# Kernel optimization log

Measured on AMD Instinct MI355X. Metric: run time of the kernel, lower is better.

Reference implementation:

```python
import jax, jax.numpy as jnp
import numpy as np

B = 32          # batch_size
S = 64          # num_subgraph
D = 8           # dim_multi_hot (module-level global in source repo)
NE = S * D      # num_edges = 512
NNODES = 1024
E = 150000      # incidence rows
IN_UNITS = [16, 32, 32]
OUT_UNITS = [32, 32, 16]


def _glorot(key, shape):
    # glorot_normal over last two dims (out, in)
    fan_out, fan_in = shape[-2], shape[-1]
    std = (2.0 / (fan_in + fan_out)) ** 0.5
    return std * jax.random.normal(key, shape, dtype=jnp.float32)


def setup_inputs() -> dict:
    key = jax.random.key(0)
    ks = jax.random.split(key, 10)
    nodes_features = jax.random.normal(ks[0], (NNODES * S, IN_UNITS[0]), dtype=jnp.float32)
    c0 = jax.random.randint(ks[1], (E,), 0, B, dtype=jnp.int32)
    c1 = jax.random.randint(ks[2], (E,), 0, NNODES, dtype=jnp.int32)
    c2 = jax.random.randint(ks[3], (E,), 0, S, dtype=jnp.int32)
    c3 = jax.random.randint(ks[4], (E,), 0, D, dtype=jnp.int32)
    incidence_matrix = jnp.stack([c0, c1, c2, c3], axis=1)
    return {
        'nodes_features': nodes_features,
        'in_core0': _glorot(ks[5], (NE, IN_UNITS[1], IN_UNITS[0])),
        'in_bias0': jnp.zeros((NE, IN_UNITS[1], 1), jnp.float32),
        'in_core1': _glorot(ks[6], (NE, IN_UNITS[2], IN_UNITS[1])),
        'in_bias1': jnp.zeros((NE, IN_UNITS[2], 1), jnp.float32),
        'out_core0': _glorot(ks[7], (NE, OUT_UNITS[1], OUT_UNITS[0])),
        'out_bias0': jnp.zeros((NE, OUT_UNITS[1], 1), jnp.float32),
        'out_core1': _glorot(ks[8], (NE, OUT_UNITS[2], OUT_UNITS[1])),
        'out_bias1': jnp.zeros((NE, OUT_UNITS[2], 1), jnp.float32),
        'incidence_matrix': incidence_matrix,
    }


def reference(nodes_features, in_core0, in_bias0, in_core1, in_bias1,
              out_core0, out_bias0, out_core1, out_bias1, incidence_matrix):
    c0 = incidence_matrix[:, 0]
    c1 = incidence_matrix[:, 1]
    c2 = incidence_matrix[:, 2]
    c3 = incidence_matrix[:, 3]

    # gather node features per incidence row: [E, in0]
    x = nodes_features[c1 * S + c2]
    eidx = c2 * D + c3  # per-edge weight index, < NE

    # per-edge MLP (gathered batched matmul + bias + relu)
    for W, b in ((in_core0, in_bias0), (in_core1, in_bias1)):
        x = jax.nn.relu(jnp.einsum('eoi,ei->eo', W[eidx], x) + b[eidx, :, 0])

    # unsorted segment mean over irregular edge groups
    seg = c0 * (D * S) + c2 * D + c3
    nseg = B * S * D
    sums = jax.ops.segment_sum(x, seg, num_segments=nseg)           # [B*NE, 32]
    cnt = jax.ops.segment_sum(jnp.ones((x.shape[0], 1), x.dtype), seg, num_segments=nseg)
    ef = jnp.where(cnt > 0, sums / jnp.maximum(cnt, 1.0), 0.0)       # [B*NE, 32]

    # output MLP: weights tiled over batch (einsum avoids explicit repeat)
    ef = ef.reshape(B, NE, -1)
    for W, b in ((out_core0, out_bias0), (out_core1, out_bias1)):
        ef = jax.nn.relu(jnp.einsum('eoi,bei->beo', W, ef) + b[None, :, :, 0])

    return ef.reshape(B * NE, OUT_UNITS[-1], 1)
```

## Files before the change

### kernel.cpp

```cpp
#include <hip/hip_runtime.h>

#define B_    32
#define S_    64
#define D_    8
#define NE_   512
#define E_    150000
#define CAP   448

#define SBLK  1024
#define BLKN  ((E_ + SBLK - 1) / SBLK)
#define SLOTS 16
#define PBIN_PITCH (BLKN * SLOTS)

#define PAYLOAD_BYTE_OFF (NE_ * BLKN * 4)

typedef __attribute__((ext_vector_type(8)))  short  short8;
typedef __attribute__((ext_vector_type(16))) float  float16;

__device__ __forceinline__ unsigned short f2bf(float f) {
    union { float f; unsigned int u; } cv; cv.f = f;
    unsigned int u = cv.u;
    return (unsigned short)((u + 0x7fffu + ((u >> 16) & 1u)) >> 16);
}
__device__ __forceinline__ unsigned int pack2bf(float a, float b) {
    return (unsigned int)f2bf(a) | ((unsigned int)f2bf(b) << 16);
}

__global__ __launch_bounds__(SBLK)
void scatter_bin(const int* __restrict__ inc,
                 int* __restrict__ cnt2D,
                 int* __restrict__ payload2D) {
    __shared__ int lcount[NE_];
    const int tid = threadIdx.x;

    for (int i = tid; i < NE_; i += SBLK) lcount[i] = 0;
    __syncthreads();

    const int e = blockIdx.x * SBLK + tid;
    int ei = -1, lp = 0, pl = 0;
    if (e < E_) {
        const int4 c = ((const int4*)inc)[e];
        ei = c.z * D_ + c.w;
        pl = (c.x << 16) | (c.y * S_ + c.z);
        lp = atomicAdd(&lcount[ei], 1);
    }
    if (ei >= 0 && lp < SLOTS)
        payload2D[ei * PBIN_PITCH + blockIdx.x * SLOTS + lp] = pl;
    __syncthreads();
    if (tid < NE_)
        cnt2D[tid * BLKN + blockIdx.x] = min(lcount[tid], SLOTS);
}

#define HLP 40

__global__ __launch_bounds__(512, 4)
void main_mfma(const float* __restrict__ nf,
               const float* __restrict__ iw0, const float* __restrict__ ib0,
               const float* __restrict__ iw1, const float* __restrict__ ib1,
               const float* __restrict__ ow0, const float* __restrict__ ob0,
               const float* __restrict__ ow1, const float* __restrict__ ob1,
               const int* __restrict__ cnt2D, const int* __restrict__ payload2D,
               float* __restrict__ out) {
    const int bid  = blockIdx.x;
    const int tid  = threadIdx.x;
    const int lane = tid & 63;
    const int wav  = tid >> 6;
    const int e32  = lane & 31;
    const int q    = lane >> 5;

    __shared__ float acc[32][33];
    __shared__ float hb[32][33];
    __shared__ float cnts[32];
    __shared__ float q0t[32 * 33];
    __shared__ float q1t[32 * 17];
    __shared__ float qb0s[32], qb1s[16];
    __shared__ float bias0s[32], bias1s[32];
    __shared__ int   scnt[160];
    __shared__ int   elist[CAP];
    __shared__ unsigned short Hl[8][32 * HLP];

    short8 aWa, aWb0, aWb1;
    {
        const float* wa = iw0 + (size_t)bid * 512 + e32 * 16 + q * 8;
        float4 u0 = ((const float4*)wa)[0], u1 = ((const float4*)wa)[1];
        unsigned int p[4] = { pack2bf(u0.x,u0.y), pack2bf(u0.z,u0.w),
                              pack2bf(u1.x,u1.y), pack2bf(u1.z,u1.w) };
        aWa = *(short8*)p;
    }
    {
        const float* wb = iw1 + (size_t)bid * 1024 + e32 * 32 + q * 8;
        float4 u0 = ((const float4*)wb)[0], u1 = ((const float4*)wb)[1];
        unsigned int p[4] = { pack2bf(u0.x,u0.y), pack2bf(u0.z,u0.w),
                              pack2bf(u1.x,u1.y), pack2bf(u1.z,u1.w) };
        aWb0 = *(short8*)p;
        const float* wb2 = wb + 16;
        float4 u2 = ((const float4*)wb2)[0], u3 = ((const float4*)wb2)[1];
        unsigned int p2[4] = { pack2bf(u2.x,u2.y), pack2bf(u2.z,u2.w),
                               pack2bf(u3.x,u3.y), pack2bf(u3.z,u3.w) };
        aWb1 = *(short8*)p2;
    }

    for (int i = tid; i < 1024; i += 512) {
        const int o = i >> 5, k = i & 31;
        q0t[k * 33 + o] = ow0[(size_t)bid * 1024 + i];
    }
    { const int o = tid >> 5, k = tid & 31;
      q1t[k * 17 + o] = ow1[(size_t)bid * 512 + tid]; }
    if (tid < 32)       { bias0s[tid] = ib0[bid * 32 + tid]; cnts[tid] = 0.f; }
    else if (tid < 64)  bias1s[tid - 32] = ib1[bid * 32 + (tid - 32)];
    else if (tid < 96)  qb0s[tid - 64] = ob0[bid * 32 + (tid - 64)];
    else if (tid < 112) qb1s[tid - 96] = ob1[bid * 16 + (tid - 96)];
    for (int i = tid; i < 32 * 33; i += 512) ((float*)acc)[i] = 0.f;

    if (wav == 0) {
        int base = 0;
        #pragma unroll
        for (int r = 0; r < 3; ++r) {
            const int idx = lane + 64 * r;
            int v = (idx < BLKN) ? cnt2D[bid * BLKN + idx] : 0;
            #pragma unroll
            for (int off = 1; off < 64; off <<= 1) {
                int y = __shfl_up(v, off, 64);
                if (lane >= off) v += y;
            }
            if (idx < BLKN + 13) scnt[idx] = base + v;
            base += __shfl(v, 63, 64);
        }
    }
    __syncthreads();

    float bA[16], bB[16];
    #pragma unroll
    for (int r = 0; r < 16; ++r) {
        const int o_r = (r & 3) + 8 * (r >> 2) + 4 * q;
        bA[r] = bias0s[o_r];
        bB[r] = bias1s[o_r];
    }

    const int n = min(scnt[BLKN - 1], CAP);

    const int* Pb = payload2D + (size_t)bid * PBIN_PITCH;
    for (int pair = tid; pair < PBIN_PITCH; pair += 512) {
        const int blk = pair >> 4, s = pair & (SLOTS - 1);
        const int b0 = blk ? scnt[blk - 1] : 0;
        const int cc = scnt[blk] - b0;
        if (s < cc) {
            const int idx = b0 + s;
            if (idx < CAP) elist[idx] = Pb[pair];
        }
    }
    __syncthreads();

    const int ntiles = (n + 31) >> 5;
    unsigned short* hl = Hl[wav];

    for (int t = wav; t < ntiles; t += 8) {
        const int slot  = t * 32 + e32;
        const bool valid = slot < n;
        const int cs    = valid ? slot : (n - 1);

        const int p   = elist[cs];
        const int b_e = p >> 16;
        const int row = p & 0xFFFF;

        short8 bX;
        {
            const float4* xp = (const float4*)(nf + (size_t)row * 16 + q * 8);
            float4 u0 = xp[0], u1 = xp[1];
            unsigned int pk[4] = { pack2bf(u0.x,u0.y), pack2bf(u0.z,u0.w),
                                   pack2bf(u1.x,u1.y), pack2bf(u1.z,u1.w) };
            bX = *(short8*)pk;
        }

        float16 c0;
        #pragma unroll
        for (int r = 0; r < 16; ++r) c0[r] = bA[r];
        c0 = __builtin_amdgcn_mfma_f32_32x32x16_bf16(aWa, bX, c0, 0, 0, 0);

        #pragma unroll
        for (int r = 0; r < 16; r += 2) {
            const int o_r = (r & 3) + 8 * (r >> 2) + 4 * q;
            const unsigned int pk = pack2bf(fmaxf(c0[r], 0.f), fmaxf(c0[r + 1], 0.f));
            *(unsigned int*)(hl + e32 * HLP + o_r) = pk;
        }

        short8 bH0 = *(const short8*)(hl + e32 * HLP + q * 8);
        short8 bH1 = *(const short8*)(hl + e32 * HLP + 16 + q * 8);
        float16 c1;
        #pragma unroll
        for (int r = 0; r < 16; ++r) c1[r] = bB[r];
        c1 = __builtin_amdgcn_mfma_f32_32x32x16_bf16(aWb0, bH0, c1, 0, 0, 0);
        c1 = __builtin_amdgcn_mfma_f32_32x32x16_bf16(aWb1, bH1, c1, 0, 0, 0);

        if (valid) {
            #pragma unroll
            for (int r = 0; r < 16; ++r) {
                const int o_r = (r & 3) + 8 * (r >> 2) + 4 * q;
                atomicAdd(&acc[b_e][o_r], fmaxf(c1[r], 0.f));
            }
            if (q == 0) atomicAdd(&cnts[b_e], 1.f);
        }
    }
    __syncthreads();

    {
        const int b  = tid >> 4;
        const int j  = tid & 15;
        const float cv  = cnts[b];
        const float inv = cv > 0.f ? 1.0f / cv : 0.0f;
        #pragma unroll
        for (int s = 0; s < 2; ++s) {
            const int oo = j * 2 + s;
            float d = 0.f;
            #pragma unroll
            for (int k = 0; k < 32; ++k) d = fmaf(q0t[k * 33 + oo], acc[b][k], d);
            hb[b][oo] = fmaxf(fmaf(d, inv, qb0s[oo]), 0.f);
        }
    }
    __syncthreads();

    {
        const int b = tid >> 4;
        const int o = tid & 15;
        float d = qb1s[o];
        #pragma unroll
        for (int k = 0; k < 32; ++k) d = fmaf(q1t[k * 17 + o], hb[b][k], d);
        out[((size_t)b * NE_ + bid) * 16 + o] = fmaxf(d, 0.f);
    }
}

extern "C" void kernel_launch(void* const* d_in, const int* in_sizes, int n_in,
                              void* d_out, int out_size, void* d_ws, size_t ws_size,
                              hipStream_t stream) {
    const float* nf  = (const float*)d_in[0];
    const float* iw0 = (const float*)d_in[1];
    const float* ib0 = (const float*)d_in[2];
    const float* iw1 = (const float*)d_in[3];
    const float* ib1 = (const float*)d_in[4];
    const float* ow0 = (const float*)d_in[5];
    const float* ob0 = (const float*)d_in[6];
    const float* ow1 = (const float*)d_in[7];
    const float* ob1 = (const float*)d_in[8];
    const int*   inc = (const int*)d_in[9];

    int* cnt2D     = (int*)d_ws;
    int* payload2D = (int*)((char*)d_ws + PAYLOAD_BYTE_OFF);

    scatter_bin<<<BLKN, SBLK, 0, stream>>>(inc, cnt2D, payload2D);
    main_mfma<<<NE_, 512, 0, stream>>>(nf, iw0, ib0, iw1, ib1, ow0, ob0, ow1, ob1,
                                       cnt2D, payload2D, (float*)d_out);
}
```

Baseline: 118.0 us.

## Fuse scatter and per-edge MLP into one cooperative kernel with grid sync

Merges the binning kernel and the main MFMA kernel into a single cooperative launch of 512 blocks that separates the phases with a grid-wide barrier, falling back to two launches if the cooperative launch fails. Scatter now uses 512 threads that each handle two incidence rows. The LDS round-trip for repacking the layer-0 activations into MFMA B operands is replaced by cross-lane shuffles, and shared memory is consolidated into one struct that reuses the edge list as the scatter counter. The aim is to remove the second launch, the inter-kernel gap and LDS traffic, at the cost of grid-sync overhead and requiring all 512 blocks to be co-resident (launch bounds lowered to 2 blocks per CU).

```diff
diff --git a/kernel.cpp b/kernel.cpp
--- a/kernel.cpp
+++ b/kernel.cpp
@@ -1,4 +1,6 @@
 #include <hip/hip_runtime.h>
+#include <hip/hip_cooperative_groups.h>
+namespace cg = cooperative_groups;
 
 #define B_    32
 #define S_    64
@@ -7,8 +9,8 @@
 #define E_    150000
 #define CAP   448
 
-#define SBLK  1024
-#define BLKN  ((E_ + SBLK - 1) / SBLK)
+#define SEPB  1024
+#define BLKN  ((E_ + SEPB - 1) / SEPB)
 #define SLOTS 16
 #define PBIN_PITCH (BLKN * SLOTS)
 
@@ -26,69 +28,65 @@
     return (unsigned int)f2bf(a) | ((unsigned int)f2bf(b) << 16);
 }
 
-__global__ __launch_bounds__(SBLK)
-void scatter_bin(const int* __restrict__ inc,
-                 int* __restrict__ cnt2D,
-                 int* __restrict__ payload2D) {
-    __shared__ int lcount[NE_];
-    const int tid = threadIdx.x;
-
-    for (int i = tid; i < NE_; i += SBLK) lcount[i] = 0;
-    __syncthreads();
-
-    const int e = blockIdx.x * SBLK + tid;
-    int ei = -1, lp = 0, pl = 0;
-    if (e < E_) {
-        const int4 c = ((const int4*)inc)[e];
-        ei = c.z * D_ + c.w;
-        pl = (c.x << 16) | (c.y * S_ + c.z);
-        lp = atomicAdd(&lcount[ei], 1);
-    }
-    if (ei >= 0 && lp < SLOTS)
-        payload2D[ei * PBIN_PITCH + blockIdx.x * SLOTS + lp] = pl;
-    __syncthreads();
-    if (tid < NE_)
-        cnt2D[tid * BLKN + blockIdx.x] = min(lcount[tid], SLOTS);
-}
-
-#define HLP 40
-
-__global__ __launch_bounds__(512, 4)
-void main_mfma(const float* __restrict__ nf,
-               const float* __restrict__ iw0, const float* __restrict__ ib0,
-               const float* __restrict__ iw1, const float* __restrict__ ib1,
-               const float* __restrict__ ow0, const float* __restrict__ ob0,
-               const float* __restrict__ ow1, const float* __restrict__ ob1,
-               const int* __restrict__ cnt2D, const int* __restrict__ payload2D,
-               float* __restrict__ out) {
-    const int bid  = blockIdx.x;
-    const int tid  = threadIdx.x;
+struct Smem {
+    int   ibuf[NE_];
+    float acc[32][33];
+    float hb[32][33];
+    float cnts[32];
+    float q0t[32 * 33];
+    float q1t[32 * 17];
+    float qb0s[32], qb1s[16];
+    float bias0s[32], bias1s[32];
+    int   scnt[160];
+};
+
+__device__ __forceinline__ void scatter_phase(int bid, int tid,
+                                              const int* __restrict__ inc,
+                                              int* __restrict__ cnt2D,
+                                              int* __restrict__ payload2D,
+                                              int* __restrict__ lcount) {
+    lcount[tid] = 0;
+    __syncthreads();
+    #pragma unroll
+    for (int r = 0; r < 2; ++r) {
+        const int e = bid * SEPB + r * 512 + tid;
+        if (e < E_) {
+            const int4 c = ((const int4*)inc)[e];
+            const int ei = c.z * D_ + c.w;
+            const int pl = (c.x << 16) | (c.y * S_ + c.z);
+            const int lp = atomicAdd(&lcount[ei], 1);
+            if (lp < SLOTS)
+                payload2D[ei * PBIN_PITCH + bid * SLOTS + lp] = pl;
+        }
+    }
+    __syncthreads();
+    cnt2D[tid * BLKN + bid] = min(lcount[tid], SLOTS);
+}
+
+__device__ __forceinline__ void process_bin(
+        int eidx, int tid,
+        const float* __restrict__ nf,
+        const float* __restrict__ iw0, const float* __restrict__ ib0,
+        const float* __restrict__ iw1, const float* __restrict__ ib1,
+        const float* __restrict__ ow0, const float* __restrict__ ob0,
+        const float* __restrict__ ow1, const float* __restrict__ ob1,
+        const int* __restrict__ cnt2D, const int* __restrict__ payload2D,
+        float* __restrict__ out, Smem& s) {
     const int lane = tid & 63;
     const int wav  = tid >> 6;
     const int e32  = lane & 31;
     const int q    = lane >> 5;
 
-    __shared__ float acc[32][33];
-    __shared__ float hb[32][33];
-    __shared__ float cnts[32];
-    __shared__ float q0t[32 * 33];
-    __shared__ float q1t[32 * 17];
-    __shared__ float qb0s[32], qb1s[16];
-    __shared__ float bias0s[32], bias1s[32];
-    __shared__ int   scnt[160];
-    __shared__ int   elist[CAP];
-    __shared__ unsigned short Hl[8][32 * HLP];
-
     short8 aWa, aWb0, aWb1;
     {
-        const float* wa = iw0 + (size_t)bid * 512 + e32 * 16 + q * 8;
+        const float* wa = iw0 + (size_t)eidx * 512 + e32 * 16 + q * 8;
         float4 u0 = ((const float4*)wa)[0], u1 = ((const float4*)wa)[1];
         unsigned int p[4] = { pack2bf(u0.x,u0.y), pack2bf(u0.z,u0.w),
                               pack2bf(u1.x,u1.y), pack2bf(u1.z,u1.w) };
         aWa = *(short8*)p;
     }
     {
-        const float* wb = iw1 + (size_t)bid * 1024 + e32 * 32 + q * 8;
+        const float* wb = iw1 + (size_t)eidx * 1024 + e32 * 32 + q * 8;
         float4 u0 = ((const float4*)wb)[0], u1 = ((const float4*)wb)[1];
         unsigned int p[4] = { pack2bf(u0.x,u0.y), pack2bf(u0.z,u0.w),
                               pack2bf(u1.x,u1.y), pack2bf(u1.z,u1.w) };
@@ -102,28 +100,28 @@
 
     for (int i = tid; i < 1024; i += 512) {
         const int o = i >> 5, k = i & 31;
-        q0t[k * 33 + o] = ow0[(size_t)bid * 1024 + i];
+        s.q0t[k * 33 + o] = ow0[(size_t)eidx * 1024 + i];
     }
     { const int o = tid >> 5, k = tid & 31;
-      q1t[k * 17 + o] = ow1[(size_t)bid * 512 + tid]; }
-    if (tid < 32)       { bias0s[tid] = ib0[bid * 32 + tid]; cnts[tid] = 0.f; }
-    else if (tid < 64)  bias1s[tid - 32] = ib1[bid * 32 + (tid - 32)];
-    else if (tid < 96)  qb0s[tid - 64] = ob0[bid * 32 + (tid - 64)];
-    else if (tid < 112) qb1s[tid - 96] = ob1[bid * 16 + (tid - 96)];
-    for (int i = tid; i < 32 * 33; i += 512) ((float*)acc)[i] = 0.f;
+      s.q1t[k * 17 + o] = ow1[(size_t)eidx * 512 + tid]; }
+    if (tid < 32)       { s.bias0s[tid] = ib0[eidx * 32 + tid]; s.cnts[tid] = 0.f; }
+    else if (tid < 64)  s.bias1s[tid - 32] = ib1[eidx * 32 + (tid - 32)];
+    else if (tid < 96)  s.qb0s[tid - 64] = ob0[eidx * 32 + (tid - 64)];
+    else if (tid < 112) s.qb1s[tid - 96] = ob1[eidx * 16 + (tid - 96)];
+    for (int i = tid; i < 32 * 33; i += 512) ((float*)s.acc)[i] = 0.f;
 
     if (wav == 0) {
         int base = 0;
         #pragma unroll
         for (int r = 0; r < 3; ++r) {
             const int idx = lane + 64 * r;
-            int v = (idx < BLKN) ? cnt2D[bid * BLKN + idx] : 0;
+            int v = (idx < BLKN) ? cnt2D[eidx * BLKN + idx] : 0;
             #pragma unroll
             for (int off = 1; off < 64; off <<= 1) {
                 int y = __shfl_up(v, off, 64);
                 if (lane >= off) v += y;
             }
-            if (idx < BLKN + 13) scnt[idx] = base + v;
+            if (idx < BLKN + 13) s.scnt[idx] = base + v;
             base += __shfl(v, 63, 64);
         }
     }
@@ -133,33 +131,31 @@
     #pragma unroll
     for (int r = 0; r < 16; ++r) {
         const int o_r = (r & 3) + 8 * (r >> 2) + 4 * q;
-        bA[r] = bias0s[o_r];
-        bB[r] = bias1s[o_r];
-    }
-
-    const int n = min(scnt[BLKN - 1], CAP);
-
-    const int* Pb = payload2D + (size_t)bid * PBIN_PITCH;
+        bA[r] = s.bias0s[o_r];
+        bB[r] = s.bias1s[o_r];
+    }
+
+    const int n = min(s.scnt[BLKN - 1], CAP);
+
+    const int* Pb = payload2D + (size_t)eidx * PBIN_PITCH;
     for (int pair = tid; pair < PBIN_PITCH; pair += 512) {
-        const int blk = pair >> 4, s = pair & (SLOTS - 1);
-        const int b0 = blk ? scnt[blk - 1] : 0;
-        const int cc = scnt[blk] - b0;
-        if (s < cc) {
-            const int idx = b0 + s;
-            if (idx < CAP) elist[idx] = Pb[pair];
+        const int blk = pair >> 4, sl = pair & (SLOTS - 1);
+        const int b0 = blk ? s.scnt[blk - 1] : 0;
+        const int cc = s.scnt[blk] - b0;
+        if (sl < cc) {
+            const int idx = b0 + sl;
+            if (idx < CAP) s.ibuf[idx] = Pb[pair];
         }
     }
     __syncthreads();
 
     const int ntiles = (n + 31) >> 5;
-    unsigned short* hl = Hl[wav];
-
     for (int t = wav; t < ntiles; t += 8) {
         const int slot  = t * 32 + e32;
         const bool valid = slot < n;
         const int cs    = valid ? slot : (n - 1);
 
-        const int p   = elist[cs];
+        const int p   = s.ibuf[cs];
         const int b_e = p >> 16;
         const int row = p & 0xFFFF;
 
@@ -177,15 +173,22 @@
         for (int r = 0; r < 16; ++r) c0[r] = bA[r];
         c0 = __builtin_amdgcn_mfma_f32_32x32x16_bf16(aWa, bX, c0, 0, 0, 0);
 
-        #pragma unroll
-        for (int r = 0; r < 16; r += 2) {
-            const int o_r = (r & 3) + 8 * (r >> 2) + 4 * q;
-            const unsigned int pk = pack2bf(fmaxf(c0[r], 0.f), fmaxf(c0[r + 1], 0.f));
-            *(unsigned int*)(hl + e32 * HLP + o_r) = pk;
-        }
-
-        short8 bH0 = *(const short8*)(hl + e32 * HLP + q * 8);
-        short8 bH1 = *(const short8*)(hl + e32 * HLP + 16 + q * 8);
+        float v[16];
+        #pragma unroll
+        for (int r = 0; r < 16; ++r) v[r] = fmaxf(c0[r], 0.f);
+        unsigned int A0 = pack2bf(v[0], v[1]),  B0 = pack2bf(v[2], v[3]);
+        unsigned int C0 = pack2bf(v[4], v[5]),  D0 = pack2bf(v[6], v[7]);
+        unsigned int A1 = pack2bf(v[8], v[9]),  B1 = pack2bf(v[10], v[11]);
+        unsigned int C1 = pack2bf(v[12], v[13]), D1 = pack2bf(v[14], v[15]);
+        unsigned int g0 = __shfl_xor(q ? A0 : C0, 32, 64);
+        unsigned int g1 = __shfl_xor(q ? B0 : D0, 32, 64);
+        unsigned int g2 = __shfl_xor(q ? A1 : C1, 32, 64);
+        unsigned int g3 = __shfl_xor(q ? B1 : D1, 32, 64);
+        unsigned int f0[4] = { q ? g0 : A0, q ? g1 : B0, q ? C0 : g0, q ? D0 : g1 };
+        unsigned int f1[4] = { q ? g2 : A1, q ? g3 : B1, q ? C1 : g2, q ? D1 : g3 };
+        short8 bH0 = *(short8*)f0;
+        short8 bH1 = *(short8*)f1;
+
         float16 c1;
         #pragma unroll
         for (int r = 0; r < 16; ++r) c1[r] = bB[r];
@@ -196,9 +199,9 @@
             #pragma unroll
             for (int r = 0; r < 16; ++r) {
                 const int o_r = (r & 3) + 8 * (r >> 2) + 4 * q;
-                atomicAdd(&acc[b_e][o_r], fmaxf(c1[r], 0.f));
+                atomicAdd(&s.acc[b_e][o_r], fmaxf(c1[r], 0.f));
             }
-            if (q == 0) atomicAdd(&cnts[b_e], 1.f);
+            if (q == 0) atomicAdd(&s.cnts[b_e], 1.f);
         }
     }
     __syncthreads();
@@ -206,15 +209,15 @@
     {
         const int b  = tid >> 4;
         const int j  = tid & 15;
-        const float cv  = cnts[b];
+        const float cv  = s.cnts[b];
         const float inv = cv > 0.f ? 1.0f / cv : 0.0f;
         #pragma unroll
-        for (int s = 0; s < 2; ++s) {
-            const int oo = j * 2 + s;
+        for (int t2 = 0; t2 < 2; ++t2) {
+            const int oo = j * 2 + t2;
             float d = 0.f;
             #pragma unroll
-            for (int k = 0; k < 32; ++k) d = fmaf(q0t[k * 33 + oo], acc[b][k], d);
-            hb[b][oo] = fmaxf(fmaf(d, inv, qb0s[oo]), 0.f);
+            for (int k = 0; k < 32; ++k) d = fmaf(s.q0t[k * 33 + oo], s.acc[b][k], d);
+            s.hb[b][oo] = fmaxf(fmaf(d, inv, s.qb0s[oo]), 0.f);
         }
     }
     __syncthreads();
@@ -222,11 +225,50 @@
     {
         const int b = tid >> 4;
         const int o = tid & 15;
-        float d = qb1s[o];
-        #pragma unroll
-        for (int k = 0; k < 32; ++k) d = fmaf(q1t[k * 17 + o], hb[b][k], d);
-        out[((size_t)b * NE_ + bid) * 16 + o] = fmaxf(d, 0.f);
-    }
+        float d = s.qb1s[o];
+        #pragma unroll
+        for (int k = 0; k < 32; ++k) d = fmaf(s.q1t[k * 17 + o], s.hb[b][k], d);
+        out[((size_t)b * NE_ + eidx) * 16 + o] = fmaxf(d, 0.f);
+    }
+}
+
+__global__ __launch_bounds__(512, 2)
+void fused_all(const float* __restrict__ nf,
+               const float* __restrict__ iw0, const float* __restrict__ ib0,
+               const float* __restrict__ iw1, const float* __restrict__ ib1,
+               const float* __restrict__ ow0, const float* __restrict__ ob0,
+               const float* __restrict__ ow1, const float* __restrict__ ob1,
+               const int* __restrict__ inc,
+               int* __restrict__ cnt2D, int* __restrict__ payload2D,
+               float* __restrict__ out) {
+    __shared__ Smem s;
+    const int bid = blockIdx.x, tid = threadIdx.x;
+    cg::grid_group grid = cg::this_grid();
+    if (bid < BLKN)
+        scatter_phase(bid, tid, inc, cnt2D, payload2D, s.ibuf);
+    grid.sync();
+    process_bin(bid, tid, nf, iw0, ib0, iw1, ib1, ow0, ob0, ow1, ob1,
+                cnt2D, payload2D, out, s);
+}
+
+__global__ __launch_bounds__(512)
+void scatter_k(const int* __restrict__ inc, int* __restrict__ cnt2D,
+               int* __restrict__ payload2D) {
+    __shared__ int lcount[NE_];
+    scatter_phase(blockIdx.x, threadIdx.x, inc, cnt2D, payload2D, lcount);
+}
+
+__global__ __launch_bounds__(512, 2)
+void main_k(const float* __restrict__ nf,
+            const float* __restrict__ iw0, const float* __restrict__ ib0,
+            const float* __restrict__ iw1, const float* __restrict__ ib1,
+            const float* __restrict__ ow0, const float* __restrict__ ob0,
+            const float* __restrict__ ow1, const float* __restrict__ ob1,
+            const int* __restrict__ cnt2D, const int* __restrict__ payload2D,
+            float* __restrict__ out) {
+    __shared__ Smem s;
+    process_bin(blockIdx.x, threadIdx.x, nf, iw0, ib0, iw1, ib1, ow0, ob0, ow1, ob1,
+                cnt2D, payload2D, out, s);
 }
 
 extern "C" void kernel_launch(void* const* d_in, const int* in_sizes, int n_in,
@@ -245,8 +287,15 @@
 
     int* cnt2D     = (int*)d_ws;
     int* payload2D = (int*)((char*)d_ws + PAYLOAD_BYTE_OFF);
-
-    scatter_bin<<<BLKN, SBLK, 0, stream>>>(inc, cnt2D, payload2D);
-    main_mfma<<<NE_, 512, 0, stream>>>(nf, iw0, ib0, iw1, ib1, ow0, ob0, ow1, ob1,
-                                       cnt2D, payload2D, (float*)d_out);
-}
+    float* out     = (float*)d_out;
+
+    void* args[] = { &nf, &iw0, &ib0, &iw1, &ib1, &ow0, &ob0, &ow1, &ob1,
+                     &inc, &cnt2D, &payload2D, &out };
+    hipError_t err = hipLaunchCooperativeKernel((const void*)fused_all,
+                                                dim3(NE_), dim3(512), args, 0, stream);
+    if (err != hipSuccess) {
+        scatter_k<<<BLKN, 512, 0, stream>>>(inc, cnt2D, payload2D);
+        main_k<<<NE_, 512, 0, stream>>>(nf, iw0, ib0, iw1, ib1, ow0, ob0, ow1, ob1,
+                                        cnt2D, payload2D, out);
+    }
+}
```

New measurement: 205.3 us. 74.0% more time.
